# Kernel optimization log

Measured on AMD Instinct MI355X. Metric: run time of the kernel, lower is better.

Reference implementation:

```python
import jax, jax.numpy as jnp
import numpy as np

B, N, C, K, E = 8, 20000, 128, 64, 320000


def setup_inputs() -> dict:
    key = jax.random.key(0)
    ks = jax.random.split(key, 8)
    x = jax.random.normal(ks[0], (B, N, C), dtype=jnp.float32)
    edge_index = jax.random.randint(ks[1], (B, 2, E), 0, N, dtype=jnp.int64)
    edge_weight = jax.random.uniform(ks[2], (B, E), dtype=jnp.float32)
    mask = jax.random.randint(ks[3], (B, N), 0, 2, dtype=jnp.int32)
    W1 = jax.random.normal(ks[4], (C, K), dtype=jnp.float32) * (1.0 / np.sqrt(C))
    b1 = jnp.zeros((K,), dtype=jnp.float32)
    W2 = jax.random.normal(ks[5], (K, K), dtype=jnp.float32) * (1.0 / np.sqrt(K))
    b2 = jnp.zeros((K,), dtype=jnp.float32)
    return {"x": x, "edge_index": edge_index, "edge_weight": edge_weight,
            "mask": mask, "W1": W1, "b1": b1, "W2": W2, "b2": b2}


def _forward(x, edge_index, edge_weight, mask, W1, b1, W2, b2):
    # x: [B,N,C]; edge_index: [B,2,E]; edge_weight: [B,E]; mask: [B,N]
    m = (mask > 0).astype(x.dtype)                         # [B,N] valid-node mask
    # assignment MLP + per-node softmax over out_nodes, zeroed for invalid nodes
    h = jax.nn.relu(jnp.einsum('bnc,ck->bnk', x, W1) + b1)
    S = jax.nn.softmax(jnp.einsum('bnk,kl->bnl', h, W2) + b2, axis=-1)
    S = S * m[..., None]                                   # [B,N,K]
    # pooled features: S^T x over valid nodes (S already masked)
    pfeat = jnp.einsum('bnk,bnc->bkc', S, x)               # [B,K,C]
    u = edge_index[:, 0]                                   # [B,E]
    v = edge_index[:, 1]                                   # [B,E]
    # edge valid iff both endpoints valid
    evalid = jnp.take_along_axis(m, u, axis=1) * jnp.take_along_axis(m, v, axis=1)
    w = edge_weight * evalid                               # [B,E]
    S_u = jnp.take_along_axis(S, u[..., None], axis=1)     # [B,E,K] gather rows
    src = w[..., None] * S_u                               # [B,E,K]
    # mid[v] += w * S[u]  (scatter-add over edges, per graph)
    mid = jax.vmap(lambda vv, ss: jnp.zeros((N, K), x.dtype).at[vv].add(ss))(v, src)
    pooled_adj = jnp.einsum('bnk,bnl->bkl', S, mid)        # [B,K,K]
    pmask = (jnp.sum(m, axis=-1, keepdims=True) > 0).astype(x.dtype) * jnp.ones((K,), x.dtype)
    return pfeat, pooled_adj, pmask


def reference(x, edge_index, edge_weight, mask, W1, b1, W2, b2):
    return _forward(x, edge_index, edge_weight, mask, W1, b1, W2, b2)
```

## Files before the change

### kernel.cpp

```cpp
#include <hip/hip_runtime.h>

#define Bb 8
#define Nn 20000
#define Cc 128
#define Kk 64
#define Ee 320000

#define WAVES_PER_BLOCK 4
#define NSEG 128
#define SEGCAP 2560

#define CS_BLOCKS 1250
#define CP_BLOCKS 256
#define PL_BLOCKS 256
#define PF_BLOCKS 512

typedef __attribute__((ext_vector_type(8))) short bf16x8;
typedef __attribute__((ext_vector_type(16))) float f32x16;

__device__ __forceinline__ unsigned short f2bf(float f) {
    unsigned int u = __float_as_uint(f);
    u += 0x7FFFu + ((u >> 16) & 1u);
    return (unsigned short)(u >> 16);
}
__device__ __forceinline__ float bf2f(unsigned int bits16) {
    return __uint_as_float(bits16 << 16);
}

__global__ __launch_bounds__(256) void k_init(
    const float* __restrict__ W1, const float* __restrict__ W2,
    const int* __restrict__ mask,
    unsigned short* __restrict__ Wf, unsigned int* __restrict__ bmg,
    float* __restrict__ pmask)
{
    __shared__ int s_any;
    const int tid = threadIdx.x;

    if (blockIdx.x == 0) {
        for (int idx = tid; idx < 8192; idx += 256) {
            const int j  = idx & 7;
            const int ln = (idx >> 3) & 63;
            const int t  = idx >> 9;
            const int kh = t & 1;
            const int cs = t >> 1;
            Wf[idx] = f2bf(W1[(cs * 16 + (ln >> 5) * 8 + j) * Kk + kh * 32 + (ln & 31)]);
        }
        for (int idx = tid; idx < 4096; idx += 256) {
            const int j  = idx & 7;
            const int ln = (idx >> 3) & 63;
            const int t  = idx >> 9;
            const int lh = t & 1;
            const int ks = t >> 1;
            Wf[8192 + idx] = f2bf(W2[(ks * 16 + (ln >> 5) * 8 + j) * Kk + lh * 32 + (ln & 31)]);
        }
        return;
    }

    const int bid  = blockIdx.x - 1;
    const int lane = tid & 63;
    const int wid  = tid >> 6;
    const int b    = bid & 7;
    const int part = bid >> 3;
    if (tid == 0) s_any = 0;
    __syncthreads();

    const int* mb = mask + (size_t)b * Nn;
    int any = 0;
    for (int g = part * 4 + wid; g < 313; g += 32) {
        const int i = g * 64 + lane;
        const bool mv = (i < Nn) ? (mb[i] > 0) : false;
        const unsigned long long mk = __ballot(mv);
        if (lane == 0) {
            bmg[b * 626 + 2 * g]     = (unsigned int)mk;
            bmg[b * 626 + 2 * g + 1] = (unsigned int)(mk >> 32);
        }
        any |= (mk != 0ull) ? 1 : 0;
    }
    if (any) atomicOr(&s_any, 1);
    __syncthreads();
    if (s_any && tid < Kk) pmask[(size_t)b * Kk + tid] = 1.f;
}

__global__ __launch_bounds__(256) void k_mid(
    const float* __restrict__ x, const int* __restrict__ mask,
    const unsigned short* __restrict__ Wf,
    const float* __restrict__ b1, const float* __restrict__ b2,
    unsigned int* __restrict__ Sh,
    const int* __restrict__ ei, const float* __restrict__ ew,
    const unsigned int* __restrict__ bmg,
    int* __restrict__ uvp, float* __restrict__ eww, int* __restrict__ cnt)
{
    __shared__ float b1s[Kk];
    __shared__ float b2s[Kk];
    __shared__ unsigned int bm[626];

    const int tid  = threadIdx.x;
    const int lane = tid & 63;
    const int wid  = tid >> 6;

    if (blockIdx.x < CS_BLOCKS) {
        if (tid < Kk) { b1s[tid] = b1[tid]; b2s[tid] = b2[tid]; }
        __syncthreads();

        const int hsel = lane >> 5;
        const int m32  = lane & 31;

        const int wc = blockIdx.x * WAVES_PER_BLOCK + wid;
        const int chunksPerBatch = Nn / 32;
        const int b  = wc / chunksPerBatch;
        const int n0 = (wc % chunksPerBatch) * 32;
        const int nd = n0 + m32;

        const unsigned short* W1A = Wf;
        const unsigned short* W2A = Wf + 8192;

        const float* xrow = x + ((size_t)b * Nn + nd) * Cc;
        f32x16 accA = 0.f, accB = 0.f;
        #pragma unroll
        for (int cs = 0; cs < 8; ++cs) {
            const float4 f0 = *(const float4*)&xrow[cs * 16 + hsel * 8];
            const float4 f1 = *(const float4*)&xrow[cs * 16 + hsel * 8 + 4];
            bf16x8 xa;
            xa[0] = (short)f2bf(f0.x); xa[1] = (short)f2bf(f0.y);
            xa[2] = (short)f2bf(f0.z); xa[3] = (short)f2bf(f0.w);
            xa[4] = (short)f2bf(f1.x); xa[5] = (short)f2bf(f1.y);
            xa[6] = (short)f2bf(f1.z); xa[7] = (short)f2bf(f1.w);
            const bf16x8 w1h0 = *(const bf16x8*)&W1A[((cs * 2 + 0) * 64 + lane) * 8];
            const bf16x8 w1h1 = *(const bf16x8*)&W1A[((cs * 2 + 1) * 64 + lane) * 8];
            accA = __builtin_amdgcn_mfma_f32_32x32x16_bf16(w1h0, xa, accA, 0, 0, 0);
            accB = __builtin_amdgcn_mfma_f32_32x32x16_bf16(w1h1, xa, accB, 0, 0, 0);
        }

        f32x16 accS0 = 0.f, accS1 = 0.f;

#define EXTRACT_GEMM2(KS, ACC)                                                 \
        {                                                                      \
            bf16x8 hf;                                                         \
            _Pragma("unroll")                                                  \
            for (int jj = 0; jj < 4; ++jj) {                                   \
                const int c0 = jj + 8 * ((KS) & 1);                            \
                const float own  = hsel ? (ACC)[c0 + 4] : (ACC)[c0];           \
                const float send = hsel ? (ACC)[c0]     : (ACC)[c0 + 4];       \
                const float sw   = __shfl_xor(send, 32);                       \
                const float vlo  = hsel ? sw  : own;                           \
                const float vhi  = hsel ? own : sw;                            \
                const int klo = (KS) * 16 + 8 * hsel + jj;                     \
                hf[jj]     = (short)f2bf(fmaxf(vlo + b1s[klo], 0.f));          \
                hf[jj + 4] = (short)f2bf(fmaxf(vhi + b1s[klo + 4], 0.f));      \
            }                                                                  \
            const bf16x8 w2l0 = *(const bf16x8*)&W2A[(((KS) * 2 + 0) * 64 + lane) * 8]; \
            const bf16x8 w2l1 = *(const bf16x8*)&W2A[(((KS) * 2 + 1) * 64 + lane) * 8]; \
            accS0 = __builtin_amdgcn_mfma_f32_32x32x16_bf16(w2l0, hf, accS0, 0, 0, 0); \
            accS1 = __builtin_amdgcn_mfma_f32_32x32x16_bf16(w2l1, hf, accS1, 0, 0, 0); \
        }

        EXTRACT_GEMM2(0, accA)
        EXTRACT_GEMM2(1, accA)
        EXTRACT_GEMM2(2, accB)
        EXTRACT_GEMM2(3, accB)
#undef EXTRACT_GEMM2

        float z0[16], z1[16];
        float mm = -1e30f;
        #pragma unroll
        for (int r = 0; r < 16; ++r) {
            const int l = (r & 3) + 8 * (r >> 2) + 4 * hsel;
            z0[r] = accS0[r] + b2s[l];
            z1[r] = accS1[r] + b2s[l + 32];
            mm = fmaxf(mm, fmaxf(z0[r], z1[r]));
        }
        mm = fmaxf(mm, __shfl_xor(mm, 32));
        float ssum = 0.f;
        #pragma unroll
        for (int r = 0; r < 16; ++r) {
            z0[r] = __expf(z0[r] - mm);
            z1[r] = __expf(z1[r] - mm);
            ssum += z0[r] + z1[r];
        }
        ssum += __shfl_xor(ssum, 32);
        const int   mv = mask[(size_t)b * Nn + nd];
        const float rs = (mv > 0) ? (1.f / ssum) : 0.f;

        unsigned int* ShRow = Sh + ((size_t)b * Nn + nd) * 32;
        #pragma unroll
        for (int g = 0; g < 4; ++g) {
            uint4 pk;
            pk.x = (unsigned int)f2bf(z0[4*g+0]*rs) | ((unsigned int)f2bf(z1[4*g+0]*rs) << 16);
            pk.y = (unsigned int)f2bf(z0[4*g+1]*rs) | ((unsigned int)f2bf(z1[4*g+1]*rs) << 16);
            pk.z = (unsigned int)f2bf(z0[4*g+2]*rs) | ((unsigned int)f2bf(z1[4*g+2]*rs) << 16);
            pk.w = (unsigned int)f2bf(z0[4*g+3]*rs) | ((unsigned int)f2bf(z1[4*g+3]*rs) << 16);
            *(uint4*)&ShRow[8 * g + 4 * hsel] = pk;
        }
        return;
    }

    const int cbid = blockIdx.x - CS_BLOCKS;
    const int b    = cbid & 7;
    const int seg  = (cbid >> 3) * 4 + wid;
    const int groupsPerBatch = Ee / 64;
    const size_t eib = (size_t)b * 2 * Ee;
    const float* ewb = ew + (size_t)b * Ee;
    int*   uvs  = uvp + ((size_t)b * NSEG + seg) * SEGCAP;
    float* ewws = eww + ((size_t)b * NSEG + seg) * SEGCAP;

    for (int i = tid; i < 626; i += 256) bm[i] = bmg[b * 626 + i];
    __syncthreads();

    int run = 0;
    for (int g = seg; g < groupsPerBatch; g += 8 * NSEG) {
        int u8[8], v8[8]; float w8[8]; int has[8];
        #pragma unroll
        for (int t = 0; t < 8; ++t) {
            const int gg = g + t * NSEG;
            has[t] = (gg < groupsPerBatch);
            const int e0 = (has[t] ? gg : g) * 64;
            u8[t] = ei[eib + e0 + lane];
            v8[t] = ei[eib + Ee + e0 + lane];
            w8[t] = ewb[e0 + lane];
        }
        #pragma unroll
        for (int t = 0; t < 8; ++t) {
            if (!has[t]) continue;
            const unsigned int uu = (unsigned int)u8[t];
            const unsigned int vv = (unsigned int)v8[t];
            const bool valid = ((bm[uu >> 5] >> (uu & 31)) & 1u) &&
                               ((bm[vv >> 5] >> (vv & 31)) & 1u);
            const unsigned long long mk = __ballot(valid);
            const int myoff = __popcll(mk & ((1ull << lane) - 1ull));
            if (valid) {
                uvs[run + myoff]  = u8[t] | (v8[t] << 15);
                ewws[run + myoff] = w8[t];
            }
            run += (int)__popcll(mk);
        }
    }
    const int ncp = (run + 31) & ~31;
    if (lane < ncp - run) { uvs[run + lane] = 0; ewws[run + lane] = 0.f; }
    if (lane == 0) cnt[b * NSEG + seg] = ncp;
}

template<bool USE_PT>
__global__ __launch_bounds__(256, 1) void k_big(
    const unsigned int* __restrict__ Sh, const int* __restrict__ uvp,
    const float* __restrict__ eww, const int* __restrict__ cnt,
    float* __restrict__ out,
    const float* __restrict__ x, float* __restrict__ pfeat)
{
    __shared__ float tile[Kk * Kk];
    const int tid  = threadIdx.x;
    const int lane = tid & 63;
    const int wid  = tid >> 6;
    const int hsel = lane >> 5;
    const int m32  = lane & 31;

    if (blockIdx.x < PL_BLOCKS) {
        for (int i = tid; i < Kk * Kk; i += 256) tile[i] = 0.f;
        __syncthreads();

        const int b   = blockIdx.x & 7;
        const int seg = (blockIdx.x >> 3) * 4 + wid;
        const unsigned int* Shb = Sh + (size_t)b * Nn * 32;
        const int*   uvs  = uvp + ((size_t)b * NSEG + seg) * SEGCAP;
        const float* ewws = eww + ((size_t)b * NSEG + seg) * SEGCAP;
        const int nc = cnt[b * NSEG + seg];

        f32x16 acc00 = 0.f, acc01 = 0.f, acc10 = 0.f, acc11 = 0.f;

#define LOADUV(UV, WW, BASE)                                        \
        _Pragma("unroll")                                           \
        for (int j = 0; j < 8; ++j) {                               \
            int sidx = (BASE) + hsel * 8 + j;                       \
            sidx = (sidx < nc) ? sidx : (nc - 1);                   \
            (UV)[j] = uvs[sidx];                                    \
            (WW)[j] = ewws[sidx];                                   \
        }

#define GATHER(GV, GU, UV)                                          \
        _Pragma("unroll")                                           \
        for (int j = 0; j < 8; ++j) {                               \
            const int uu = (UV)[j] & 32767;                         \
            const int vv = ((UV)[j] >> 15) & 32767;                 \
            (GV)[j] = Shb[(size_t)vv * 32 + m32];                   \
            (GU)[j] = Shb[(size_t)uu * 32 + m32];                   \
        }

#define CONSUME(GV, GU, WW)                                         \
        {                                                           \
            bf16x8 a0, a1, b0, b1;                                  \
            _Pragma("unroll")                                       \
            for (int j = 0; j < 8; ++j) {                           \
                a0[j] = (short)f2bf((WW)[j] * bf2f((GV)[j] & 0xffffu)); \
                a1[j] = (short)f2bf((WW)[j] * bf2f((GV)[j] >> 16)); \
                b0[j] = (short)((GU)[j] & 0xffffu);                 \
                b1[j] = (short)((GU)[j] >> 16);                     \
            }                                                       \
            acc00 = __builtin_amdgcn_mfma_f32_32x32x16_bf16(a0, b0, acc00, 0, 0, 0); \
            acc01 = __builtin_amdgcn_mfma_f32_32x32x16_bf16(a0, b1, acc01, 0, 0, 0); \
            acc10 = __builtin_amdgcn_mfma_f32_32x32x16_bf16(a1, b0, acc10, 0, 0, 0); \
            acc11 = __builtin_amdgcn_mfma_f32_32x32x16_bf16(a1, b1, acc11, 0, 0, 0); \
        }

        if (nc > 0) {
            int uvA[8], uvB[8];
            float wwA[8], wwB[8];
            unsigned int gvA[8], guA[8], gvB[8], guB[8];

            LOADUV(uvA, wwA, 0)
            GATHER(gvA, guA, uvA)
            LOADUV(uvB, wwB, 16)

            for (int c0 = 0; c0 < nc; c0 += 32) {
                GATHER(gvB, guB, uvB)
                int uvA2[8], uvB2[8]; float wwA2[8], wwB2[8];
                LOADUV(uvA2, wwA2, c0 + 32)
                LOADUV(uvB2, wwB2, c0 + 48)
                CONSUME(gvA, guA, wwA)
                GATHER(gvA, guA, uvA2)
                CONSUME(gvB, guB, wwB)
                #pragma unroll
                for (int j = 0; j < 8; ++j) {
                    uvB[j] = uvB2[j]; wwB[j] = wwB2[j]; wwA[j] = wwA2[j];
                }
            }
        }
#undef LOADUV
#undef GATHER
#undef CONSUME

        const int rbase = 4 * (lane >> 5);
        const int col   = lane & 31;
        #pragma unroll
        for (int r = 0; r < 16; ++r) {
            const int row = (r & 3) + 8 * (r >> 2) + rbase;
            atomicAdd(&tile[row * Kk + col],              acc00[r]);
            atomicAdd(&tile[row * Kk + 32 + col],         acc01[r]);
            atomicAdd(&tile[(32 + row) * Kk + col],       acc10[r]);
            atomicAdd(&tile[(32 + row) * Kk + 32 + col],  acc11[r]);
        }
        __syncthreads();

        if (USE_PT) {
            float* pt = out + (size_t)blockIdx.x * (Kk * Kk);
            for (int i = tid; i < Kk * Kk; i += 256) pt[i] = tile[i];
        } else {
            float* pb = out + (size_t)b * Kk * Kk;
            for (int i = tid; i < Kk * Kk; i += 256) atomicAdd(&pb[i], tile[i]);
        }
        return;
    }

    const int pbid = blockIdx.x - PL_BLOCKS;
    const int b    = pbid & 7;
    const int slot = pbid >> 3;
    const int bpb  = PF_BLOCKS >> 3;

    const float* xb = x + (size_t)b * Nn * Cc;
    const unsigned int* Shb = Sh + (size_t)b * Nn * 32;

    const int nodeoff = (lane >> 5) * 8;
    const int kc      = lane & 31;
    const int c       = wid * 32 + kc;

    f32x16 acc0 = 0.f, acc1 = 0.f;

    const int chunks = Nn / 16;
    for (int ch = slot; ch < chunks; ch += bpb) {
        const int nb = ch * 16 + nodeoff;
        unsigned int g[8]; float bff[8];
        #pragma unroll
        for (int j = 0; j < 8; ++j) {
            const size_t n = (size_t)(nb + j);
            g[j]   = Shb[n * 32 + kc];
            bff[j] = xb[n * Cc + c];
        }
        bf16x8 a0, a1, bbf;
        #pragma unroll
        for (int j = 0; j < 8; ++j) {
            a0[j]  = (short)(g[j] & 0xffffu);
            a1[j]  = (short)(g[j] >> 16);
            bbf[j] = (short)f2bf(bff[j]);
        }
        acc0 = __builtin_amdgcn_mfma_f32_32x32x16_bf16(a0, bbf, acc0, 0, 0, 0);
        acc1 = __builtin_amdgcn_mfma_f32_32x32x16_bf16(a1, bbf, acc1, 0, 0, 0);
    }

    float* pf = pfeat + (size_t)b * Kk * Cc;
    const int colc  = wid * 32 + (lane & 31);
    const int rbase = 4 * (lane >> 5);
    #pragma unroll
    for (int r = 0; r < 16; ++r) {
        const int row = (r & 3) + 8 * (r >> 2) + rbase;
        atomicAdd(&pf[row * Cc + colc],        acc0[r]);
        atomicAdd(&pf[(32 + row) * Cc + colc], acc1[r]);
    }
}

__global__ __launch_bounds__(256) void k_reduce_pooled(
    const float* __restrict__ pt, float* __restrict__ pooled)
{
    const int b    = blockIdx.x & 7;
    const int part = blockIdx.x >> 3;
    const int tid  = threadIdx.x;
    #pragma unroll
    for (int i2 = 0; i2 < 2; ++i2) {
        const int i = part * 512 + i2 * 256 + tid;
        float s = 0.f;
        #pragma unroll 8
        for (int slot = 0; slot < 32; ++slot)
            s += pt[(size_t)(slot * 8 + b) * (Kk * Kk) + i];
        pooled[(size_t)b * Kk * Kk + i] = s;
    }
}

extern "C" void kernel_launch(void* const* d_in, const int* in_sizes, int n_in,
                              void* d_out, int out_size, void* d_ws, size_t ws_size,
                              hipStream_t stream)
{
    const float* x    = (const float*)d_in[0];
    const int*   ei   = (const int*)d_in[1];
    const float* ew   = (const float*)d_in[2];
    const int*   mask = (const int*)d_in[3];
    const float* W1   = (const float*)d_in[4];
    const float* b1   = (const float*)d_in[5];
    const float* W2   = (const float*)d_in[6];
    const float* b2   = (const float*)d_in[7];

    float* out    = (float*)d_out;
    float* pfeat  = out;
    float* pooled = out + (size_t)Bb * Kk * Cc;
    float* pmask  = out + (size_t)Bb * Kk * Cc + (size_t)Bb * Kk * Kk;

    unsigned int* Sh = (unsigned int*)d_ws;
    int*   uvp  = (int*)(Sh + (size_t)Bb * Nn * 32);
    float* eww  = (float*)(uvp + (size_t)Bb * NSEG * SEGCAP);
    int*   cnt  = (int*)(eww + (size_t)Bb * NSEG * SEGCAP);
    unsigned int* bmg = (unsigned int*)(cnt + Bb * NSEG);
    unsigned short* Wf = (unsigned short*)(bmg + Bb * 626);
    float* pt   = (float*)(Wf + 12288);
    const size_t needed = (size_t)((char*)(pt + (size_t)PL_BLOCKS * Kk * Kk) - (char*)d_ws);
    const bool use_pt = ws_size >= needed;

    hipMemsetAsync(d_out, 0, sizeof(float) * (size_t)out_size, stream);

    k_init<<<65, 256, 0, stream>>>(W1, W2, mask, Wf, bmg, pmask);
    k_mid<<<CS_BLOCKS + CP_BLOCKS, 256, 0, stream>>>(
        x, mask, Wf, b1, b2, Sh, ei, ew, bmg, uvp, eww, cnt);
    if (use_pt) {
        k_big<true><<<PL_BLOCKS + PF_BLOCKS, 256, 0, stream>>>(
            Sh, uvp, eww, cnt, pt, x, pfeat);
        k_reduce_pooled<<<64, 256, 0, stream>>>(pt, pooled);
    } else {
        k_big<false><<<PL_BLOCKS + PF_BLOCKS, 256, 0, stream>>>(
            Sh, uvp, eww, cnt, pooled, x, pfeat);
    }
}
```

Before: 106.9 us.

## Deepen edge gather pipeline to three stages and drop partial-tile reduction kernel

Restructures the pooled-adjacency loop to keep three 16-edge groups in flight, so index loads and S-row gathers are issued further ahead of the MFMA consume step. Segment padding becomes a multiple of 48 and the segment capacity grows to match. It also removes the per-block partial-tile buffer and its separate reduction kernel, using global atomics into the pooled output instead. This saves one launch and a buffer round trip, but adds atomic contention and register pressure, plus extra padded work per segment.

```diff
diff --git a/kernel.cpp b/kernel.cpp
--- a/kernel.cpp
+++ b/kernel.cpp
@@ -8,7 +8,7 @@
 
 #define WAVES_PER_BLOCK 4
 #define NSEG 128
-#define SEGCAP 2560
+#define SEGCAP 2592
 
 #define CS_BLOCKS 1250
 #define CP_BLOCKS 256
@@ -234,16 +234,15 @@
             run += (int)__popcll(mk);
         }
     }
-    const int ncp = (run + 31) & ~31;
+    const int ncp = ((run + 47) / 48) * 48;
     if (lane < ncp - run) { uvs[run + lane] = 0; ewws[run + lane] = 0.f; }
     if (lane == 0) cnt[b * NSEG + seg] = ncp;
 }
 
-template<bool USE_PT>
 __global__ __launch_bounds__(256, 1) void k_big(
     const unsigned int* __restrict__ Sh, const int* __restrict__ uvp,
     const float* __restrict__ eww, const int* __restrict__ cnt,
-    float* __restrict__ out,
+    float* __restrict__ pooled,
     const float* __restrict__ x, float* __restrict__ pfeat)
 {
     __shared__ float tile[Kk * Kk];
@@ -301,25 +300,32 @@
         }
 
         if (nc > 0) {
-            int uvA[8], uvB[8];
-            float wwA[8], wwB[8];
-            unsigned int gvA[8], guA[8], gvB[8], guB[8];
+            int uvA[8], uvB[8], uvC[8];
+            float wwA[8], wwB[8], wwC[8];
+            unsigned int gvA[8], guA[8], gvB[8], guB[8], gvC[8], guC[8];
 
             LOADUV(uvA, wwA, 0)
+            LOADUV(uvB, wwB, 16)
+            LOADUV(uvC, wwC, 32)
             GATHER(gvA, guA, uvA)
-            LOADUV(uvB, wwB, 16)
-
-            for (int c0 = 0; c0 < nc; c0 += 32) {
-                GATHER(gvB, guB, uvB)
-                int uvA2[8], uvB2[8]; float wwA2[8], wwB2[8];
-                LOADUV(uvA2, wwA2, c0 + 32)
-                LOADUV(uvB2, wwB2, c0 + 48)
+            GATHER(gvB, guB, uvB)
+
+            for (int c0 = 0; c0 < nc; c0 += 48) {
+                int uvD[8], uvE[8], uvF[8];
+                float wwD[8], wwE[8], wwF[8];
+                LOADUV(uvD, wwD, c0 + 48)
+                GATHER(gvC, guC, uvC)
                 CONSUME(gvA, guA, wwA)
-                GATHER(gvA, guA, uvA2)
+                LOADUV(uvE, wwE, c0 + 64)
+                GATHER(gvA, guA, uvD)
                 CONSUME(gvB, guB, wwB)
+                LOADUV(uvF, wwF, c0 + 80)
+                GATHER(gvB, guB, uvE)
+                CONSUME(gvC, guC, wwC)
                 #pragma unroll
                 for (int j = 0; j < 8; ++j) {
-                    uvB[j] = uvB2[j]; wwB[j] = wwB2[j]; wwA[j] = wwA2[j];
+                    wwA[j] = wwD[j]; wwB[j] = wwE[j]; wwC[j] = wwF[j];
+                    uvC[j] = uvF[j];
                 }
             }
         }
@@ -339,13 +345,9 @@
         }
         __syncthreads();
 
-        if (USE_PT) {
-            float* pt = out + (size_t)blockIdx.x * (Kk * Kk);
-            for (int i = tid; i < Kk * Kk; i += 256) pt[i] = tile[i];
-        } else {
-            float* pb = out + (size_t)b * Kk * Kk;
-            for (int i = tid; i < Kk * Kk; i += 256) atomicAdd(&pb[i], tile[i]);
-        }
+        float* pb = pooled + (size_t)b * Kk * Kk;
+        for (int i = tid; i < Kk * Kk; i += 256)
+            atomicAdd(&pb[i], tile[i]);
         return;
     }
 
@@ -392,23 +394,6 @@
         const int row = (r & 3) + 8 * (r >> 2) + rbase;
         atomicAdd(&pf[row * Cc + colc],        acc0[r]);
         atomicAdd(&pf[(32 + row) * Cc + colc], acc1[r]);
-    }
-}
-
-__global__ __launch_bounds__(256) void k_reduce_pooled(
-    const float* __restrict__ pt, float* __restrict__ pooled)
-{
-    const int b    = blockIdx.x & 7;
-    const int part = blockIdx.x >> 3;
-    const int tid  = threadIdx.x;
-    #pragma unroll
-    for (int i2 = 0; i2 < 2; ++i2) {
-        const int i = part * 512 + i2 * 256 + tid;
-        float s = 0.f;
-        #pragma unroll 8
-        for (int slot = 0; slot < 32; ++slot)
-            s += pt[(size_t)(slot * 8 + b) * (Kk * Kk) + i];
-        pooled[(size_t)b * Kk * Kk + i] = s;
     }
 }
 
@@ -436,21 +421,12 @@
     int*   cnt  = (int*)(eww + (size_t)Bb * NSEG * SEGCAP);
     unsigned int* bmg = (unsigned int*)(cnt + Bb * NSEG);
     unsigned short* Wf = (unsigned short*)(bmg + Bb * 626);
-    float* pt   = (float*)(Wf + 12288);
-    const size_t needed = (size_t)((char*)(pt + (size_t)PL_BLOCKS * Kk * Kk) - (char*)d_ws);
-    const bool use_pt = ws_size >= needed;
 
     hipMemsetAsync(d_out, 0, sizeof(float) * (size_t)out_size, stream);
 
     k_init<<<65, 256, 0, stream>>>(W1, W2, mask, Wf, bmg, pmask);
     k_mid<<<CS_BLOCKS + CP_BLOCKS, 256, 0, stream>>>(
         x, mask, Wf, b1, b2, Sh, ei, ew, bmg, uvp, eww, cnt);
-    if (use_pt) {
-        k_big<true><<<PL_BLOCKS + PF_BLOCKS, 256, 0, stream>>>(
-            Sh, uvp, eww, cnt, pt, x, pfeat);
-        k_reduce_pooled<<<64, 256, 0, stream>>>(pt, pooled);
-    } else {
-        k_big<false><<<PL_BLOCKS + PF_BLOCKS, 256, 0, stream>>>(
-            Sh, uvp, eww, cnt, pooled, x, pfeat);
-    }
-}
+    k_big<<<PL_BLOCKS + PF_BLOCKS, 256, 0, stream>>>(
+        Sh, uvp, eww, cnt, pooled, x, pfeat);
+}
```

Result: no change. 105.1 us (-1.6%).
